# Optimization experiments

Measured on AMD Instinct MI355X. Metric: run time of the kernel, lower is better.

The kernel has to match this reference:

```python
import jax, jax.numpy as jnp
import numpy as np

# ---- dims (from init_kwargs) ----
B_SZ = 16; K = 1; NC = 64; NR = 4; RF = 4; L_UL = 8
M_ANT = 256; N_ANT = 1024; BS_TDD = 16; RIS_TDD = 16
FC = 100e9; BW = 1e9; UPSNR = 10.0; MAX_DELAY = 5e-9; BIT = 1
C = NC  # PSA channel = Nc


def setup_inputs():
    key = jax.random.key(0)
    ks = jax.random.split(key, 20)
    f = jnp.float32
    d = {}
    d['H_BR_re'] = jax.random.normal(ks[0], (NC, N_ANT, M_ANT), f)
    d['H_BR_im'] = jax.random.normal(ks[1], (NC, N_ANT, M_ANT), f)
    d['H_RU_re'] = jax.random.normal(ks[2], (B_SZ, K, NC, NR, N_ANT), f)
    d['H_RU_im'] = jax.random.normal(ks[3], (B_SZ, K, NC, NR, N_ANT), f)
    d['H_BU_re'] = jax.random.normal(ks[4], (B_SZ, K, NC, NR, M_ANT), f)
    d['H_BU_im'] = jax.random.normal(ks[5], (B_SZ, K, NC, NR, M_ANT), f)
    # unit complex Gaussian noise, scaled by sqrt(Power*SNR/2) inside reference
    d['noise_re'] = jax.random.normal(ks[6], (B_SZ, L_UL, NC, NR, RF), f)
    d['noise_im'] = jax.random.normal(ks[7], (B_SZ, L_UL, NC, NR, RF), f)
    # learned parameters (torch: Parameter tensors in __init__)
    d['Phase1'] = jax.random.uniform(ks[8], (L_UL, N_ANT), f)
    d['Phase2'] = jax.random.uniform(ks[9], (L_UL, N_ANT), f)
    d['Phase_TDD'] = jax.random.normal(ks[10], (L_UL, RIS_TDD), f)
    d['S_analog'] = jax.random.normal(ks[11], (L_UL, NC, M_ANT, RF), f)
    d['S_analog_TDD'] = jax.random.normal(ks[12], (L_UL, NC, BS_TDD, RF), f)
    # ParallelPolarizedSelfAttention(channel=Nc) weights (1x1 convs -> [out,in])
    s = 0.05
    d['ch_wv_w'] = jax.random.normal(ks[13], (C // 2, C), f) * s
    d['ch_wv_b'] = jnp.zeros((C // 2,), f)
    d['ch_wq_w'] = jax.random.normal(ks[14], (1, C), f) * s
    d['ch_wq_b'] = jnp.zeros((1,), f)
    d['ch_wz_w'] = jax.random.normal(ks[15], (C, C // 2), f) * s
    d['ch_wz_b'] = jnp.zeros((C,), f)
    d['ln_w'] = jnp.ones((C,), f)
    d['ln_b'] = jnp.zeros((C,), f)
    d['sp_wv_w'] = jax.random.normal(ks[16], (C // 2, C), f) * s
    d['sp_wv_b'] = jnp.zeros((C // 2,), f)
    d['sp_wq_w'] = jax.random.normal(ks[17], (C // 2, C), f) * s
    d['sp_wq_b'] = jnp.zeros((C // 2,), f)
    return d


def _conv1x1(x, w, b):
    # 1x1 conv == channel mixing
    return jnp.einsum('bchw,oc->bohw', x, w) + b[None, :, None, None]


def _psa(x, ch_wv_w, ch_wv_b, ch_wq_w, ch_wq_b, ch_wz_w, ch_wz_b, ln_w, ln_b,
         sp_wv_w, sp_wv_b, sp_wq_w, sp_wq_b):
    # Parallel Polarized Self-Attention (channel branch + spatial branch)
    b, c, h, w = x.shape
    # channel-only self-attention
    cwv = _conv1x1(x, ch_wv_w, ch_wv_b).reshape(b, c // 2, h * w)
    cwq = jax.nn.softmax(_conv1x1(x, ch_wq_w, ch_wq_b).reshape(b, h * w), axis=1)
    cwz = jnp.einsum('bkn,bn->bk', cwv, cwq)          # [b, c//2]
    z = cwz @ ch_wz_w.T + ch_wz_b                      # [b, c]
    mu = jnp.mean(z, axis=-1, keepdims=True)
    var = jnp.var(z, axis=-1, keepdims=True)
    zn = (z - mu) / jnp.sqrt(var + 1e-5) * ln_w + ln_b  # LayerNorm over channel
    ch_weight = jax.nn.sigmoid(zn)[:, :, None, None]
    # spatial-only self-attention
    swv = _conv1x1(x, sp_wv_w, sp_wv_b).reshape(b, c // 2, h * w)
    swq = jax.nn.softmax(jnp.mean(_conv1x1(x, sp_wq_w, sp_wq_b), axis=(2, 3)), axis=-1)
    swz = jnp.einsum('bk,bkn->bn', swq, swv)
    sp_weight = jax.nn.sigmoid(swz.reshape(b, 1, h, w))
    return sp_weight * x + ch_weight * x


def reference(H_BR_re, H_BR_im, H_RU_re, H_RU_im, H_BU_re, H_BU_im,
              noise_re, noise_im, Phase1, Phase2, Phase_TDD, S_analog, S_analog_TDD,
              ch_wv_w, ch_wv_b, ch_wq_w, ch_wq_b, ch_wz_w, ch_wz_b, ln_w, ln_b,
              sp_wv_w, sp_wv_b, sp_wq_w, sp_wq_b):
    H_BR = H_BR_re + 1j * H_BR_im                       # [Nc, N_ant, M_ant]
    H_RU = H_RU_re[:, K - 1] + 1j * H_RU_im[:, K - 1]   # [B, Nc, Nr, N_ant]
    H_BU = H_BU_re[:, K - 1] + 1j * H_BU_im[:, K - 1]   # [B, Nc, Nr, M_ant]
    two_pi = 2.0 * jnp.pi
    # subcarrier frequencies fm = (n - (Nc+1)/2) * B/Nc + fc
    fm = ((jnp.arange(NC, dtype=jnp.float32) + 1.0) - (NC + 1) / 2.0) * (BW / NC) + FC
    # phase quantization (bit = 1 -> seg = pi)
    seg = two_pi / (2 ** BIT)
    th1 = jnp.exp(1j * (jnp.floor(two_pi * Phase1 / seg) * seg))  # [L, N_ant]
    th2 = jnp.exp(1j * (jnp.floor(two_pi * Phase2 / seg) * seg))  # [L, N_ant]
    # RIS true-time-delay phase, kron(Phi_T, ones(1, N_ant//RIS_TDD)) == repeat
    a1 = MAX_DELAY * jax.nn.sigmoid(Phase_TDD)                    # [L, RIS_TDD]
    phi_t = jnp.exp(1j * two_pi * fm[None, :, None] * a1[:, None, :])
    phi_tdd = jnp.repeat(phi_t, N_ANT // RIS_TDD, axis=-1)        # [L, Nc, N_ant]
    theta = th1[:, None, :] * phi_tdd * th2[:, None, :]           # diag(Theta) entries
    # BS analog precoder with TTDs; kron(S_T, ones(M//BS_TDD,1)) == row repeat
    S = jnp.exp(1j * S_analog) / float(np.sqrt(M_ANT))            # [L, Nc, M, RF]
    bdel = MAX_DELAY * jax.nn.sigmoid(S_analog_TDD)               # [L, Nc, BS_TDD, RF]
    s_t = jnp.exp(1j * two_pi * fm[None, :, None, None] * bdel)
    F = S * jnp.repeat(s_t, M_ANT // BS_TDD, axis=2)              # [L, Nc, M, RF]
    # H_RU @ diag(theta) == column-wise scaling (fused, no NxN diag matmul)
    scaled = H_RU[:, None] * theta[None, :, :, None, :]           # [B, L, Nc, Nr, N_ant]
    a = jnp.einsum('blcrn,cnm->blcrm', scaled, H_BR) + H_BU[:, None]
    y0 = jnp.einsum('blcrm,lcmf->blcrf', a, F)                    # [B, L, Nc, Nr, RF]
    power = jnp.sum(jnp.abs(y0) ** 2, axis=(3, 4))[..., None, None]
    snr_lin = 10.0 ** (-UPSNR / 10.0)
    noise = (noise_re + 1j * noise_im) * jnp.sqrt(power * snr_lin / 2.0)
    y = y0 + noise
    Y = jnp.transpose(y, (0, 2, 3, 4, 1)).reshape(B_SZ, NC, K * NR * RF, L_UL)
    x = jnp.concatenate([jnp.real(Y), jnp.imag(Y)], axis=3)       # [B, Nc, K*Nr*RF, 2L]
    return _psa(x, ch_wv_w, ch_wv_b, ch_wq_w, ch_wq_b, ch_wz_w, ch_wz_b,
                ln_w, ln_b, sp_wv_w, sp_wv_b, sp_wq_w, sp_wq_b)
```

## Files before the change

### kernel.cpp

```cpp
#include <hip/hip_runtime.h>
#include <math.h>

static constexpr double TWO_PI_D = 6.283185307179586476925287;

static constexpr size_t OFF_THRE = 0;
static constexpr size_t OFF_THIM = 524288;
static constexpr size_t OFF_FBF  = 1048576;
static constexpr size_t OFF_WTBF = 1572864;
static constexpr size_t OFF_Y0P  = 3670016;
static constexpr size_t OFF_X    = 4980736;
static constexpr size_t WS_FLOATS = 5242880;

typedef __attribute__((ext_vector_type(8))) short short8;
typedef __attribute__((ext_vector_type(4))) float f32x4;

__device__ __forceinline__ double fm_of(int c){
  return ((double)(c + 1) - 32.5) * (1.0e9 / 64.0) + 1.0e11;
}
__device__ __forceinline__ unsigned short f2bf(float x){
  unsigned int u = __float_as_uint(x);
  return (unsigned short)((u + 0x7FFFu + ((u >> 16) & 1u)) >> 16);
}

__global__ __launch_bounds__(256) void k_prep(
    const float* __restrict__ P1, const float* __restrict__ P2,
    const float* __restrict__ PT, const float* __restrict__ SA,
    const float* __restrict__ ST,
    float* __restrict__ tre, float* __restrict__ tim, unsigned short* __restrict__ Fbf)
{
  __shared__ double tcs[16], tsn[16];
  int bid = blockIdx.x, tid = threadIdx.x;
  const float TWO_PI_F = 6.2831855f, SEG_F = 3.1415927f;
  if (bid < 2048){
    int l = bid >> 8, c = (bid >> 2) & 63, n0 = (bid & 3) * 256;
    if (tid < 4){
      int ris = (n0 >> 6) + tid;
      double a1 = 5.0e-9 / (1.0 + exp((double)(-PT[l * 16 + ris])));
      sincos(TWO_PI_D * fm_of(c) * a1, &tsn[tid], &tcs[tid]);
    }
    __syncthreads();
    int n = n0 + tid;
    float p1 = P1[l * 1024 + n], p2 = P2[l * 1024 + n];
    int k1 = (int)floorf((TWO_PI_F * p1) / SEG_F);
    int k2 = (int)floorf((TWO_PI_F * p2) / SEG_F);
    float s = ((k1 + k2) & 1) ? -1.f : 1.f;
    int t = (l * 64 + c) * 1024 + n;
    int ti = tid >> 6;
    tre[t] = s * (float)tcs[ti];
    tim[t] = s * (float)tsn[ti];
  } else {
    int bid2 = bid - 2048;
    int l = bid2 >> 8, c = (bid2 >> 2) & 63, f = bid2 & 3;
    int m = tid;
    if (tid < 16){
      double bdel = 5.0e-9 / (1.0 + exp((double)(-ST[((l * 64 + c) * 16 + tid) * 4 + f])));
      sincos(TWO_PI_D * fm_of(c) * bdel, &tsn[tid], &tcs[tid]);
    }
    __syncthreads();
    float sa_ = SA[(size_t)((l * 64 + c) * 256 + m) * 4 + f];
    float ssa, csa;
    sincosf(sa_, &ssa, &csa);
    float cb = (float)tcs[m >> 4], sb = (float)tsn[m >> 4];
    size_t base = ((size_t)(c * 2) * 32 + (l * 4 + f)) * 256 + m;
    Fbf[base]        = f2bf((csa * cb - ssa * sb) * 0.0625f);
    Fbf[base + 8192] = f2bf((csa * sb + ssa * cb) * 0.0625f);
  }
}

__global__ __launch_bounds__(512) void k_W(
    const float* __restrict__ Hre, const float* __restrict__ Him,
    const unsigned short* __restrict__ Fbf,
    const float* __restrict__ tre, const float* __restrict__ tim,
    unsigned short* __restrict__ WTbf)
{
  __shared__ __align__(16) short lA[2][2][256][32];
  __shared__ __align__(16) short lB[2][2][32][32];
  const int bid = blockIdx.x;
  const int c = bid >> 2, n0 = (bid & 3) * 256;
  const int tid = threadIdx.x;
  const int lane = tid & 63, w = tid >> 6;
  const int lftile = w & 1, ng = w >> 1;
  const int kq = lane >> 4, rm = lane & 15;
  const int s_mq = tid & 7, s_nr = tid >> 3;
  const int b_comp = tid >> 7, b_lf = (tid >> 2) & 31, b_q = tid & 3;

  f32x4 accRe[4], accIm[4];
  #pragma unroll
  for (int i = 0; i < 4; i++){
    accRe[i] = (f32x4){0.f, 0.f, 0.f, 0.f};
    accIm[i] = (f32x4){0.f, 0.f, 0.f, 0.f};
  }
  float4 sRe[4], sIm[4];
  short8 sB;

  auto LOADC = [&](int ck){
    size_t m0 = (size_t)ck * 32;
    #pragma unroll
    for (int p = 0; p < 4; p++){
      int n = p * 64 + s_nr;
      size_t g = ((size_t)c * 1024 + n0 + n) * 256 + m0 + s_mq * 4;
      sRe[p] = *(const float4*)(Hre + g);
      sIm[p] = *(const float4*)(Him + g);
    }
    if (tid < 256){
      size_t gb = ((size_t)(c * 2 + b_comp) * 32 + b_lf) * 256 + m0 + b_q * 8;
      sB = *(const short8*)(Fbf + gb);
    }
  };
  auto WRITEC = [&](int buf){
    #pragma unroll
    for (int p = 0; p < 4; p++){
      int n = p * 64 + s_nr;
      int eo = (((s_mq >> 1) ^ (n & 3)) << 3) + (s_mq & 1) * 4;
      unsigned int r0 = (unsigned)f2bf(sRe[p].x) | ((unsigned)f2bf(sRe[p].y) << 16);
      unsigned int r1 = (unsigned)f2bf(sRe[p].z) | ((unsigned)f2bf(sRe[p].w) << 16);
      *(uint2*)&lA[buf][0][n][eo] = make_uint2(r0, r1);
      unsigned int i0 = (unsigned)f2bf(sIm[p].x) | ((unsigned)f2bf(sIm[p].y) << 16);
      unsigned int i1 = (unsigned)f2bf(sIm[p].z) | ((unsigned)f2bf(sIm[p].w) << 16);
      *(uint2*)&lA[buf][1][n][eo] = make_uint2(i0, i1);
    }
    if (tid < 256){
      *(short8*)&lB[buf][b_comp][b_lf][(b_q ^ (b_lf & 3)) << 3] = sB;
    }
  };
  auto COMPUTE = [&](int buf){
    int col = lftile * 16 + rm;
    int be = (kq ^ (col & 3)) << 3;
    short8 bRe = *(const short8*)&lB[buf][0][col][be];
    short8 bIm = *(const short8*)&lB[buf][1][col][be];
    short8 bImN;
    #pragma unroll
    for (int i = 0; i < 8; i++) bImN[i] = bIm[i] ^ (short)0x8000;
    #pragma unroll
    for (int nt = 0; nt < 4; nt++){
      int n = ng * 64 + nt * 16 + rm;
      int eo = (kq ^ (n & 3)) << 3;
      short8 are = *(const short8*)&lA[buf][0][n][eo];
      short8 aim = *(const short8*)&lA[buf][1][n][eo];
      accRe[nt] = __builtin_amdgcn_mfma_f32_16x16x32_bf16(are, bRe,  accRe[nt], 0, 0, 0);
      accRe[nt] = __builtin_amdgcn_mfma_f32_16x16x32_bf16(aim, bImN, accRe[nt], 0, 0, 0);
      accIm[nt] = __builtin_amdgcn_mfma_f32_16x16x32_bf16(are, bIm,  accIm[nt], 0, 0, 0);
      accIm[nt] = __builtin_amdgcn_mfma_f32_16x16x32_bf16(aim, bRe,  accIm[nt], 0, 0, 0);
    }
  };

  LOADC(0); WRITEC(0); __syncthreads();
  for (int ck = 0; ck < 8; ck++){
    int buf = ck & 1;
    if (ck < 7) LOADC(ck + 1);
    COMPUTE(buf);
    if (ck < 7) WRITEC(buf ^ 1);
    __syncthreads();
  }

  const int lf = lftile * 16 + rm;
  const int l = lf >> 2;
  #pragma unroll
  for (int nt = 0; nt < 4; nt++){
    int nb = n0 + ng * 64 + nt * 16 + kq * 4;
    unsigned short pr[4], pi_[4];
    #pragma unroll
    for (int r = 0; r < 4; r++){
      size_t ti = (size_t)(l * 64 + c) * 1024 + nb + r;
      float wr = tre[ti], wi = tim[ti];
      float xr = accRe[nt][r], xi = accIm[nt][r];
      pr[r]  = f2bf(wr * xr - wi * xi);
      pi_[r] = f2bf(wr * xi + wi * xr);
    }
    size_t rb = ((size_t)(c * 2) * 32 + lf) * 1024 + nb;
    *(uint2*)(WTbf + rb) =
        make_uint2((unsigned)pr[0] | ((unsigned)pr[1] << 16),
                   (unsigned)pr[2] | ((unsigned)pr[3] << 16));
    *(uint2*)(WTbf + rb + 32768) =
        make_uint2((unsigned)pi_[0] | ((unsigned)pi_[1] << 16),
                   (unsigned)pi_[2] | ((unsigned)pi_[3] << 16));
  }
}

__global__ __launch_bounds__(512) void k_y0(
    const float* __restrict__ Rre, const float* __restrict__ Rim,
    const float* __restrict__ Ure, const float* __restrict__ Uim,
    const unsigned short* __restrict__ WTbf, const unsigned short* __restrict__ Fbf,
    float* __restrict__ Y0p)
{
  __shared__ __align__(16) short lA[2][2][64][32];
  __shared__ __align__(16) short lB[2][2][32][32];
  const int bid = blockIdx.x;
  const int chunk = bid >> 6, c = bid & 63;
  const int tid = threadIdx.x;
  const int lane = tid & 63, w = tid >> 6;
  const int lftile = w & 1, mt = w >> 1;
  const int kq = lane >> 4, rm = lane & 15;
  const int s_mq = tid & 7, s_nr = tid >> 3;
  const int b_comp = tid >> 7, b_lf = (tid >> 2) & 31, b_q = tid & 3;

  const float* Are; const float* Aim; int ars, ac0;
  const unsigned short* Bb; int brs;
  if (chunk < 4){ Are = Rre; Aim = Rim; ars = 1024; ac0 = chunk * 256; Bb = WTbf; brs = 1024; }
  else          { Are = Ure; Aim = Uim; ars = 256;  ac0 = 0;           Bb = Fbf;  brs = 256;  }
  const size_t arow = ((size_t)((s_nr >> 2) * 64 + c) * 4 + (s_nr & 3)) * ars + ac0;

  f32x4 accRe = {0.f,0.f,0.f,0.f}, accIm = {0.f,0.f,0.f,0.f};
  float4 sRe, sIm; short8 sB;

  auto LOADC = [&](int ck){
    size_t g = arow + ck * 32 + s_mq * 4;
    sRe = *(const float4*)(Are + g);
    sIm = *(const float4*)(Aim + g);
    if (tid < 256){
      size_t gb = ((size_t)(c * 2 + b_comp) * 32 + b_lf) * brs + ac0 + ck * 32 + b_q * 8;
      sB = *(const short8*)(Bb + gb);
    }
  };
  auto WRITEC = [&](int buf){
    int eo = (((s_mq >> 1) ^ (s_nr & 3)) << 3) + (s_mq & 1) * 4;
    unsigned int r0 = (unsigned)f2bf(sRe.x) | ((unsigned)f2bf(sRe.y) << 16);
    unsigned int r1 = (unsigned)f2bf(sRe.z) | ((unsigned)f2bf(sRe.w) << 16);
    *(uint2*)&lA[buf][0][s_nr][eo] = make_uint2(r0, r1);
    unsigned int i0 = (unsigned)f2bf(sIm.x) | ((unsigned)f2bf(sIm.y) << 16);
    unsigned int i1 = (unsigned)f2bf(sIm.z) | ((unsigned)f2bf(sIm.w) << 16);
    *(uint2*)&lA[buf][1][s_nr][eo] = make_uint2(i0, i1);
    if (tid < 256){
      *(short8*)&lB[buf][b_comp][b_lf][(b_q ^ (b_lf & 3)) << 3] = sB;
    }
  };
  auto COMPUTE = [&](int buf){
    int col = lftile * 16 + rm;
    int be = (kq ^ (col & 3)) << 3;
    short8 bRe = *(const short8*)&lB[buf][0][col][be];
    short8 bIm = *(const short8*)&lB[buf][1][col][be];
    short8 bImN;
    #pragma unroll
    for (int i = 0; i < 8; i++) bImN[i] = bIm[i] ^ (short)0x8000;
    int row = mt * 16 + rm;
    int eo = (kq ^ (row & 3)) << 3;
    short8 are = *(const short8*)&lA[buf][0][row][eo];
    short8 aim = *(const short8*)&lA[buf][1][row][eo];
    accRe = __builtin_amdgcn_mfma_f32_16x16x32_bf16(are, bRe,  accRe, 0, 0, 0);
    accRe = __builtin_amdgcn_mfma_f32_16x16x32_bf16(aim, bImN, accRe, 0, 0, 0);
    accIm = __builtin_amdgcn_mfma_f32_16x16x32_bf16(are, bIm,  accIm, 0, 0, 0);
    accIm = __builtin_amdgcn_mfma_f32_16x16x32_bf16(aim, bRe,  accIm, 0, 0, 0);
  };

  LOADC(0); WRITEC(0); __syncthreads();
  for (int ck = 0; ck < 8; ck++){
    int buf = ck & 1;
    if (ck < 7) LOADC(ck + 1);
    COMPUTE(buf);
    if (ck < 7) WRITEC(buf ^ 1);
    __syncthreads();
  }

  #pragma unroll
  for (int r = 0; r < 4; r++){
    int row = mt * 16 + kq * 4 + r;
    int lf = lftile * 16 + rm;
    size_t idx = ((size_t)(chunk * 64 + c) * 64 + row) * 32 + lf;
    float2 o; o.x = accRe[r]; o.y = accIm[r];
    *(float2*)(Y0p + idx * 2) = o;
  }
}

__global__ __launch_bounds__(256) void k_fin(
    const float* __restrict__ Y0p,
    const float* __restrict__ nre, const float* __restrict__ nim,
    float* __restrict__ X)
{
  int wid = blockIdx.x * 4 + (threadIdx.x >> 6);
  int lane = threadIdx.x & 63;
  int c = wid & 63, l = (wid >> 6) & 7, b = wid >> 9;
  int pair = lane >> 2;
  int r = pair >> 2, f = pair & 3;
  float yR = 0.f, yI = 0.f;
  #pragma unroll
  for (int ch = 0; ch < 5; ch++){
    size_t idx = ((size_t)(ch * 64 + c) * 64 + b * 4 + r) * 32 + l * 4 + f;
    float2 v = *(const float2*)(Y0p + idx * 2);
    yR += v.x; yI += v.y;
  }
  float p = yR * yR + yI * yI;
  p += __shfl_xor(p, 4); p += __shfl_xor(p, 8);
  p += __shfl_xor(p, 16); p += __shfl_xor(p, 32);
  float sc = sqrtf(p * 0.05f);
  if ((lane & 3) == 0){
    size_t ni = ((size_t)((b * 8 + l) * 64 + c) * 4 + r) * 4 + f;
    float oR = yR + nre[ni] * sc;
    float oI = yI + nim[ni] * sc;
    size_t xb = ((size_t)(b * 64 + c) * 16 + pair) * 16;
    X[xb + l]     = oR;
    X[xb + 8 + l] = oI;
  }
}

__global__ __launch_bounds__(256) void k_psa(
    const float* __restrict__ Xin,
    const float* __restrict__ wv_w, const float* __restrict__ wv_b,
    const float* __restrict__ wq_w, const float* __restrict__ wq_b,
    const float* __restrict__ wz_w, const float* __restrict__ wz_b,
    const float* __restrict__ lnw, const float* __restrict__ lnb,
    const float* __restrict__ sv_w, const float* __restrict__ sv_b,
    const float* __restrict__ sq_w, const float* __restrict__ sq_b,
    float* __restrict__ out)
{
  __shared__ float x[64 * 257];
  __shared__ float buf[256];
  __shared__ float xms[64], xqs[64], chw[64], wcomb[64];
  __shared__ float cwzs[32], swqs[32];
  __shared__ float red4[8];
  int b = blockIdx.x, tid = threadIdx.x;
  const float* xin = Xin + (size_t)b * 16384;
  for (int kk = 0; kk < 64; kk++){
    int i = tid + 256 * kk;
    x[(i >> 8) * 257 + (i & 255)] = xin[i];
  }
  __syncthreads();
  if (tid < 64){
    float s = 0.f;
    for (int n = 0; n < 256; n++) s += x[tid * 257 + n];
    xms[tid] = s * (1.f / 256.f);
  }
  float lq = wq_b[0];
  for (int cc = 0; cc < 64; cc++) lq += wq_w[cc] * x[cc * 257 + tid];
  float mx = lq;
  for (int s = 1; s < 64; s <<= 1) mx = fmaxf(mx, __shfl_xor(mx, s));
  if ((tid & 63) == 0) red4[tid >> 6] = mx;
  __syncthreads();
  mx = fmaxf(fmaxf(red4[0], red4[1]), fmaxf(red4[2], red4[3]));
  float e = expf(lq - mx);
  float se = e;
  for (int s = 1; s < 64; s <<= 1) se += __shfl_xor(se, s);
  if ((tid & 63) == 0) red4[4 + (tid >> 6)] = se;
  __syncthreads();
  se = red4[4] + red4[5] + red4[6] + red4[7];
  buf[tid] = e / se;
  __syncthreads();
  if (tid < 64){
    float s = 0.f;
    for (int n = 0; n < 256; n++) s += x[tid * 257 + n] * buf[n];
    xqs[tid] = s;
  }
  __syncthreads();
  if (tid < 32){
    float s = wv_b[tid];
    for (int cc = 0; cc < 64; cc++) s += wv_w[tid * 64 + cc] * xqs[cc];
    cwzs[tid] = s;
  }
  __syncthreads();
  if (tid < 64){
    float z = wz_b[tid];
    for (int k = 0; k < 32; k++) z += cwzs[k] * wz_w[tid * 32 + k];
    float s1 = z, s2 = z * z;
    for (int s = 1; s < 64; s <<= 1){ s1 += __shfl_xor(s1, s); s2 += __shfl_xor(s2, s); }
    float mu = s1 * (1.f / 64.f);
    float var = s2 * (1.f / 64.f) - mu * mu;
    float zn = (z - mu) * rsqrtf(var + 1e-5f) * lnw[tid] + lnb[tid];
    chw[tid] = 1.f / (1.f + expf(-zn));
  }
  if (tid < 32){
    float s = sq_b[tid];
    for (int cc = 0; cc < 64; cc++) s += sq_w[tid * 64 + cc] * xms[cc];
    float m2 = s;
    for (int st = 1; st < 32; st <<= 1) m2 = fmaxf(m2, __shfl_xor(m2, st));
    float ee = expf(s - m2), ss = ee;
    for (int st = 1; st < 32; st <<= 1) ss += __shfl_xor(ss, st);
    swqs[tid] = ee / ss;
  }
  __syncthreads();
  if (tid < 64){
    float s = 0.f;
    for (int k = 0; k < 32; k++) s += swqs[k] * sv_w[k * 64 + tid];
    wcomb[tid] = s;
  }
  __syncthreads();
  float bcomb = 0.f;
  for (int k = 0; k < 32; k++) bcomb += swqs[k] * sv_b[k];
  float sz = bcomb;
  for (int cc = 0; cc < 64; cc++) sz += wcomb[cc] * x[cc * 257 + tid];
  float spw = 1.f / (1.f + expf(-sz));
  buf[tid] = spw;
  __syncthreads();
  for (int kk = 0; kk < 64; kk++){
    int i = tid + 256 * kk;
    int cc = i >> 8, n = i & 255;
    out[(size_t)b * 16384 + i] = (buf[n] + chw[cc]) * x[cc * 257 + n];
  }
}

extern "C" void kernel_launch(void* const* d_in, const int* in_sizes, int n_in,
                              void* d_out, int out_size, void* d_ws, size_t ws_size,
                              hipStream_t stream)
{
  if (ws_size < WS_FLOATS * sizeof(float)) return;
  const float* HBRre = (const float*)d_in[0];
  const float* HBRim = (const float*)d_in[1];
  const float* HRUre = (const float*)d_in[2];
  const float* HRUim = (const float*)d_in[3];
  const float* HBUre = (const float*)d_in[4];
  const float* HBUim = (const float*)d_in[5];
  const float* nre   = (const float*)d_in[6];
  const float* nim   = (const float*)d_in[7];
  const float* P1    = (const float*)d_in[8];
  const float* P2    = (const float*)d_in[9];
  const float* PT    = (const float*)d_in[10];
  const float* SA    = (const float*)d_in[11];
  const float* ST    = (const float*)d_in[12];
  const float* wv_w  = (const float*)d_in[13];
  const float* wv_b  = (const float*)d_in[14];
  const float* wq_w  = (const float*)d_in[15];
  const float* wq_b  = (const float*)d_in[16];
  const float* wz_w  = (const float*)d_in[17];
  const float* wz_b  = (const float*)d_in[18];
  const float* lnw   = (const float*)d_in[19];
  const float* lnb   = (const float*)d_in[20];
  const float* sv_w  = (const float*)d_in[21];
  const float* sv_b  = (const float*)d_in[22];
  const float* sq_w  = (const float*)d_in[23];
  const float* sq_b  = (const float*)d_in[24];

  float* ws  = (float*)d_ws;
  float* tre = ws + OFF_THRE;
  float* tim = ws + OFF_THIM;
  unsigned short* fbf  = (unsigned short*)(ws + OFF_FBF);
  unsigned short* wtbf = (unsigned short*)(ws + OFF_WTBF);
  float* y0p = ws + OFF_Y0P;
  float* xb  = ws + OFF_X;

  k_prep<<<4096, 256, 0, stream>>>(P1, P2, PT, SA, ST, tre, tim, fbf);
  k_W<<<256, 512, 0, stream>>>(HBRre, HBRim, fbf, tre, tim, wtbf);
  k_y0<<<320, 512, 0, stream>>>(HRUre, HRUim, HBUre, HBUim, wtbf, fbf, y0p);
  k_fin<<<2048, 256, 0, stream>>>(y0p, nre, nim, xb);
  k_psa<<<16, 256, 0, stream>>>(xb, wv_w, wv_b, wq_w, wq_b, wz_w, wz_b,
                                lnw, lnb, sv_w, sv_b, sq_w, sq_b, (float*)d_out);
}
```

Measured before the change: 61.75 us.

## Rewrite k_W to load MFMA operands directly from global, dropping LDS staging

The W-product kernel stops staging H_BR and F tiles through double-buffered shared memory with barriers. Each wave now loads its bf16 MFMA fragments straight from global memory into registers, converting to bf16 on the fly. The grid grows from 256 to 1024 blocks of 256 threads, each covering 64 antenna rows instead of 256, to raise parallelism for this memory-bound stage. In exchange, F fragments are reloaded redundantly by every wave, and global reads use strided 32-byte segments per lane instead of coalesced tile loads.

```diff
diff --git a/kernel.cpp b/kernel.cpp
--- a/kernel.cpp
+++ b/kernel.cpp
@@ -67,107 +67,79 @@
   }
 }
 
-__global__ __launch_bounds__(512) void k_W(
+__global__ __launch_bounds__(256) void k_W(
     const float* __restrict__ Hre, const float* __restrict__ Him,
     const unsigned short* __restrict__ Fbf,
     const float* __restrict__ tre, const float* __restrict__ tim,
     unsigned short* __restrict__ WTbf)
 {
-  __shared__ __align__(16) short lA[2][2][256][32];
-  __shared__ __align__(16) short lB[2][2][32][32];
   const int bid = blockIdx.x;
-  const int c = bid >> 2, n0 = (bid & 3) * 256;
-  const int tid = threadIdx.x;
-  const int lane = tid & 63, w = tid >> 6;
-  const int lftile = w & 1, ng = w >> 1;
+  const int c = bid >> 4;
+  const int n0 = (bid & 15) * 64;
+  const int lane = threadIdx.x & 63, w = threadIdx.x >> 6;
+  const int nt = n0 + w * 16;
   const int kq = lane >> 4, rm = lane & 15;
-  const int s_mq = tid & 7, s_nr = tid >> 3;
-  const int b_comp = tid >> 7, b_lf = (tid >> 2) & 31, b_q = tid & 3;
-
-  f32x4 accRe[4], accIm[4];
+
+  const size_t arow = ((size_t)c * 1024 + nt + rm) * 256 + kq * 8;
+  const float* hr = Hre + arow;
+  const float* hi = Him + arow;
+  const unsigned short* f0 = Fbf + (size_t)(c * 2) * 8192 + kq * 8;
+  const unsigned short* fr0 = f0 + rm * 256;
+  const unsigned short* fi0 = fr0 + 8192;
+  const unsigned short* fr1 = f0 + (16 + rm) * 256;
+  const unsigned short* fi1 = fr1 + 8192;
+
+  f32x4 accRe0 = {0.f,0.f,0.f,0.f}, accIm0 = {0.f,0.f,0.f,0.f};
+  f32x4 accRe1 = {0.f,0.f,0.f,0.f}, accIm1 = {0.f,0.f,0.f,0.f};
+
   #pragma unroll
-  for (int i = 0; i < 4; i++){
-    accRe[i] = (f32x4){0.f, 0.f, 0.f, 0.f};
-    accIm[i] = (f32x4){0.f, 0.f, 0.f, 0.f};
-  }
-  float4 sRe[4], sIm[4];
-  short8 sB;
-
-  auto LOADC = [&](int ck){
-    size_t m0 = (size_t)ck * 32;
+  for (int ck = 0; ck < 8; ck++){
+    const int mo = ck * 32;
+    float4 r0 = *(const float4*)(hr + mo);
+    float4 r1 = *(const float4*)(hr + mo + 4);
+    float4 i0 = *(const float4*)(hi + mo);
+    float4 i1 = *(const float4*)(hi + mo + 4);
+    short8 bRe0 = *(const short8*)(fr0 + mo);
+    short8 bIm0 = *(const short8*)(fi0 + mo);
+    short8 bRe1 = *(const short8*)(fr1 + mo);
+    short8 bIm1 = *(const short8*)(fi1 + mo);
+    short8 are, aim;
+    are[0]=(short)f2bf(r0.x); are[1]=(short)f2bf(r0.y); are[2]=(short)f2bf(r0.z); are[3]=(short)f2bf(r0.w);
+    are[4]=(short)f2bf(r1.x); are[5]=(short)f2bf(r1.y); are[6]=(short)f2bf(r1.z); are[7]=(short)f2bf(r1.w);
+    aim[0]=(short)f2bf(i0.x); aim[1]=(short)f2bf(i0.y); aim[2]=(short)f2bf(i0.z); aim[3]=(short)f2bf(i0.w);
+    aim[4]=(short)f2bf(i1.x); aim[5]=(short)f2bf(i1.y); aim[6]=(short)f2bf(i1.z); aim[7]=(short)f2bf(i1.w);
+    short8 bImN0, bImN1;
     #pragma unroll
-    for (int p = 0; p < 4; p++){
-      int n = p * 64 + s_nr;
-      size_t g = ((size_t)c * 1024 + n0 + n) * 256 + m0 + s_mq * 4;
-      sRe[p] = *(const float4*)(Hre + g);
-      sIm[p] = *(const float4*)(Him + g);
-    }
-    if (tid < 256){
-      size_t gb = ((size_t)(c * 2 + b_comp) * 32 + b_lf) * 256 + m0 + b_q * 8;
-      sB = *(const short8*)(Fbf + gb);
-    }
-  };
-  auto WRITEC = [&](int buf){
-    #pragma unroll
-    for (int p = 0; p < 4; p++){
-      int n = p * 64 + s_nr;
-      int eo = (((s_mq >> 1) ^ (n & 3)) << 3) + (s_mq & 1) * 4;
-      unsigned int r0 = (unsigned)f2bf(sRe[p].x) | ((unsigned)f2bf(sRe[p].y) << 16);
-      unsigned int r1 = (unsigned)f2bf(sRe[p].z) | ((unsigned)f2bf(sRe[p].w) << 16);
-      *(uint2*)&lA[buf][0][n][eo] = make_uint2(r0, r1);
-      unsigned int i0 = (unsigned)f2bf(sIm[p].x) | ((unsigned)f2bf(sIm[p].y) << 16);
-      unsigned int i1 = (unsigned)f2bf(sIm[p].z) | ((unsigned)f2bf(sIm[p].w) << 16);
-      *(uint2*)&lA[buf][1][n][eo] = make_uint2(i0, i1);
-    }
-    if (tid < 256){
-      *(short8*)&lB[buf][b_comp][b_lf][(b_q ^ (b_lf & 3)) << 3] = sB;
-    }
-  };
-  auto COMPUTE = [&](int buf){
-    int col = lftile * 16 + rm;
-    int be = (kq ^ (col & 3)) << 3;
-    short8 bRe = *(const short8*)&lB[buf][0][col][be];
-    short8 bIm = *(const short8*)&lB[buf][1][col][be];
-    short8 bImN;
-    #pragma unroll
-    for (int i = 0; i < 8; i++) bImN[i] = bIm[i] ^ (short)0x8000;
-    #pragma unroll
-    for (int nt = 0; nt < 4; nt++){
-      int n = ng * 64 + nt * 16 + rm;
-      int eo = (kq ^ (n & 3)) << 3;
-      short8 are = *(const short8*)&lA[buf][0][n][eo];
-      short8 aim = *(const short8*)&lA[buf][1][n][eo];
-      accRe[nt] = __builtin_amdgcn_mfma_f32_16x16x32_bf16(are, bRe,  accRe[nt], 0, 0, 0);
-      accRe[nt] = __builtin_amdgcn_mfma_f32_16x16x32_bf16(aim, bImN, accRe[nt], 0, 0, 0);
-      accIm[nt] = __builtin_amdgcn_mfma_f32_16x16x32_bf16(are, bIm,  accIm[nt], 0, 0, 0);
-      accIm[nt] = __builtin_amdgcn_mfma_f32_16x16x32_bf16(aim, bRe,  accIm[nt], 0, 0, 0);
-    }
-  };
-
-  LOADC(0); WRITEC(0); __syncthreads();
-  for (int ck = 0; ck < 8; ck++){
-    int buf = ck & 1;
-    if (ck < 7) LOADC(ck + 1);
-    COMPUTE(buf);
-    if (ck < 7) WRITEC(buf ^ 1);
-    __syncthreads();
-  }
-
-  const int lf = lftile * 16 + rm;
-  const int l = lf >> 2;
+    for (int j = 0; j < 8; j++){
+      bImN0[j] = bIm0[j] ^ (short)0x8000;
+      bImN1[j] = bIm1[j] ^ (short)0x8000;
+    }
+    accRe0 = __builtin_amdgcn_mfma_f32_16x16x32_bf16(are, bRe0,  accRe0, 0, 0, 0);
+    accRe0 = __builtin_amdgcn_mfma_f32_16x16x32_bf16(aim, bImN0, accRe0, 0, 0, 0);
+    accIm0 = __builtin_amdgcn_mfma_f32_16x16x32_bf16(are, bIm0,  accIm0, 0, 0, 0);
+    accIm0 = __builtin_amdgcn_mfma_f32_16x16x32_bf16(aim, bRe0,  accIm0, 0, 0, 0);
+    accRe1 = __builtin_amdgcn_mfma_f32_16x16x32_bf16(are, bRe1,  accRe1, 0, 0, 0);
+    accRe1 = __builtin_amdgcn_mfma_f32_16x16x32_bf16(aim, bImN1, accRe1, 0, 0, 0);
+    accIm1 = __builtin_amdgcn_mfma_f32_16x16x32_bf16(are, bIm1,  accIm1, 0, 0, 0);
+    accIm1 = __builtin_amdgcn_mfma_f32_16x16x32_bf16(aim, bRe1,  accIm1, 0, 0, 0);
+  }
+
   #pragma unroll
-  for (int nt = 0; nt < 4; nt++){
-    int nb = n0 + ng * 64 + nt * 16 + kq * 4;
+  for (int t = 0; t < 2; t++){
+    const f32x4 aR = t ? accRe1 : accRe0;
+    const f32x4 aI = t ? accIm1 : accIm0;
+    int lf = t * 16 + rm;
+    int l = lf >> 2;
     unsigned short pr[4], pi_[4];
     #pragma unroll
     for (int r = 0; r < 4; r++){
-      size_t ti = (size_t)(l * 64 + c) * 1024 + nb + r;
+      size_t ti = (size_t)(l * 64 + c) * 1024 + nt + kq * 4 + r;
       float wr = tre[ti], wi = tim[ti];
-      float xr = accRe[nt][r], xi = accIm[nt][r];
+      float xr = aR[r], xi = aI[r];
       pr[r]  = f2bf(wr * xr - wi * xi);
       pi_[r] = f2bf(wr * xi + wi * xr);
     }
-    size_t rb = ((size_t)(c * 2) * 32 + lf) * 1024 + nb;
+    size_t rb = ((size_t)(c * 2) * 32 + lf) * 1024 + nt + kq * 4;
     *(uint2*)(WTbf + rb) =
         make_uint2((unsigned)pr[0] | ((unsigned)pr[1] << 16),
                    (unsigned)pr[2] | ((unsigned)pr[3] << 16));
@@ -426,7 +398,7 @@
   float* xb  = ws + OFF_X;
 
   k_prep<<<4096, 256, 0, stream>>>(P1, P2, PT, SA, ST, tre, tim, fbf);
-  k_W<<<256, 512, 0, stream>>>(HBRre, HBRim, fbf, tre, tim, wtbf);
+  k_W<<<1024, 256, 0, stream>>>(HBRre, HBRim, fbf, tre, tim, wtbf);
   k_y0<<<320, 512, 0, stream>>>(HRUre, HRUim, HBUre, HBUim, wtbf, fbf, y0p);
   k_fin<<<2048, 256, 0, stream>>>(y0p, nre, nim, xb);
   k_psa<<<16, 256, 0, stream>>>(xb, wv_w, wv_b, wq_w, wq_b, wz_w, wz_b,
```

New measurement: 69.98 us. 13.3% more time.
